# Performance work log

Hardware: AMD Instinct MI355X
Metric: run time of the kernel (lower is better)

## Reference

```python
import jax, jax.numpy as jnp
import numpy as np

N_HEADS = 16
EMBED = 1024
HEAD = EMBED // N_HEADS


def setup_inputs() -> dict:
    key = jax.random.key(0)
    k1, k2, k3, k4, k5 = jax.random.split(key, 5)
    x = jax.random.normal(k1, (2, 2048, EMBED), dtype=jnp.float32)
    # nn.Linear params: weight [out, in], bias [out]
    s_in = 1.0 / np.sqrt(EMBED)
    W_qkv = jax.random.uniform(k2, (3 * EMBED, EMBED), minval=-s_in, maxval=s_in, dtype=jnp.float32)
    b_qkv = jax.random.uniform(k3, (3 * EMBED,), minval=-s_in, maxval=s_in, dtype=jnp.float32)
    W_out = jax.random.uniform(k4, (EMBED, EMBED), minval=-s_in, maxval=s_in, dtype=jnp.float32)
    b_out = jax.random.uniform(k5, (EMBED,), minval=-s_in, maxval=s_in, dtype=jnp.float32)
    return {"x": x, "W_qkv": W_qkv, "b_qkv": b_qkv, "W_out": W_out, "b_out": b_out}


def reference(x, W_qkv, b_qkv, W_out, b_out):
    n, seq_len, _ = x.shape
    qkv = x @ W_qkv.T + b_qkv                       # [n, s, 3*E]
    q, k, v = jnp.split(qkv, 3, axis=2)
    def heads(t):
        return t.reshape(n, seq_len, N_HEADS, HEAD).transpose(0, 2, 1, 3)  # [n,h,s,d]
    q, k, v = heads(q), heads(k), heads(v)
    logits = jnp.einsum('bhqd,bhkd->bhqk', q, k) / jnp.sqrt(jnp.float32(HEAD))
    causal = jnp.tril(jnp.ones((seq_len, seq_len), dtype=bool))
    logits = jnp.where(causal[None, None], logits, -jnp.inf)
    attn = jax.nn.softmax(logits, axis=-1)
    o = jnp.einsum('bhqk,bhkd->bhqd', attn, v)      # [n,h,s,d]
    o = o.transpose(0, 2, 1, 3).reshape(n, seq_len, EMBED)
    return o @ W_out.T + b_out
```

## Files before the change

kernel.cpp:

```cpp
#include <hip/hip_runtime.h>
#include <hip/hip_bf16.h>
#include <stdint.h>

typedef unsigned short u16;
typedef unsigned int u32;
typedef __attribute__((ext_vector_type(8))) __bf16 bf16x8;
typedef __attribute__((ext_vector_type(8))) u16 u16x8;
typedef __attribute__((ext_vector_type(4))) u16 u16x4;
typedef __attribute__((ext_vector_type(4))) float f32x4;
typedef __attribute__((ext_vector_type(4))) u32 u32x4;
typedef __attribute__((ext_vector_type(2))) u32 u32x2;

#define S_LEN 2048
#define QSCALE 0.180336880f

__device__ __forceinline__ u16 f2bf(float f) {
  u32 u = __builtin_bit_cast(u32, f);
  u32 r = u + 0x7fffu + ((u >> 16) & 1u);
  return (u16)(r >> 16);
}
__device__ __forceinline__ float bf2f(u16 h) {
  u32 u = ((u32)h) << 16;
  return __builtin_bit_cast(float, u);
}
__device__ __forceinline__ float ex2(float x) { return __builtin_exp2f(x); }
__device__ __forceinline__ u32 cvtpk(float lo, float hi) {
  u32 d;
  asm("v_cvt_pk_bf16_f32 %0, %1, %2" : "=v"(d) : "v"(lo), "v"(hi));
  return d;
}

__device__ __forceinline__ void gload_lds16(const void* g, void* l) {
  __builtin_amdgcn_global_load_lds(
      (const __attribute__((address_space(1))) void*)g,
      (__attribute__((address_space(3))) void*)l, 16, 0, 0);
}

#define N4_X 1048576
#define N4_WQKV 786432
#define N4_WOUT 262144
__global__ void f2bf_all(const float* __restrict__ x, const float* __restrict__ wq,
                         const float* __restrict__ wo, u16* __restrict__ xb,
                         u16* __restrict__ wqb, u16* __restrict__ wob) {
  int i = blockIdx.x * blockDim.x + threadIdx.x;
  int stride = gridDim.x * blockDim.x;
  const int total = N4_X + N4_WQKV + N4_WOUT;
  for (; i < total; i += stride) {
    const float4* src; ushort4* dst; int k;
    if (i < N4_X) { src = (const float4*)x; dst = (ushort4*)xb; k = i; }
    else if (i < N4_X + N4_WQKV) { src = (const float4*)wq; dst = (ushort4*)wqb; k = i - N4_X; }
    else { src = (const float4*)wo; dst = (ushort4*)wob; k = i - N4_X - N4_WQKV; }
    float4 v = src[k];
    ushort4 o;
    o.x = f2bf(v.x); o.y = f2bf(v.y); o.z = f2bf(v.z); o.w = f2bf(v.w);
    dst[k] = o;
  }
}

template<int MODE, int XN>
__global__ __launch_bounds__(256) void gemm_bt(
    const u16* __restrict__ A, const u16* __restrict__ B,
    const float* __restrict__ bias, void* __restrict__ C0,
    u16* __restrict__ C1, int M, int N, int K, int ldc) {
  __shared__ __align__(16) u16 As[128 * 64];
  __shared__ __align__(16) u16 Bs[128 * 64];
  const int tid = threadIdx.x;
  const int wid = tid >> 6, lane = tid & 63;
  const int l15 = lane & 15, l4 = lane >> 4;
  const int wr = wid >> 1, wc = wid & 1;

  const int bid = blockIdx.x;
  const int xcd = bid & 7, s = bid >> 3;
  const int mtiles = M >> 7;
  const int nt = xcd * XN + s / mtiles;
  const int mt = s % mtiles;
  const int bm = mt * 128, bn = nt * 128;

  f32x4 acc[4][4] = {};

  for (int k0 = 0; k0 < K; k0 += 64) {
#pragma unroll
    for (int i = 0; i < 4; ++i) {
      int c = i * 256 + tid;
      int row = c >> 3, kc = c & 7;
      int sl = ((kc ^ (row & 7)) << 3);
      gload_lds16(A + (size_t)(bm + row) * K + k0 + sl, (char*)As + c * 16);
      gload_lds16(B + (size_t)(bn + row) * K + k0 + sl, (char*)Bs + c * 16);
    }
    __syncthreads();

#pragma unroll
    for (int kk = 0; kk < 2; ++kk) {
      bf16x8 a[4], b[4];
#pragma unroll
      for (int mi = 0; mi < 4; ++mi) {
        int row = wr * 64 + mi * 16 + l15;
        int slot = (kk * 4 + l4) ^ (row & 7);
        a[mi] = __builtin_bit_cast(bf16x8,
            *(const u32x4*)((char*)As + row * 128 + (slot << 4)));
      }
#pragma unroll
      for (int ni = 0; ni < 4; ++ni) {
        int row = wc * 64 + ni * 16 + l15;
        int slot = (kk * 4 + l4) ^ (row & 7);
        b[ni] = __builtin_bit_cast(bf16x8,
            *(const u32x4*)((char*)Bs + row * 128 + (slot << 4)));
      }
#pragma unroll
      for (int mi = 0; mi < 4; ++mi)
#pragma unroll
        for (int ni = 0; ni < 4; ++ni)
          acc[mi][ni] = __builtin_amdgcn_mfma_f32_16x16x32_bf16(
              a[mi], b[ni], acc[mi][ni], 0, 0, 0);
    }
    __syncthreads();
  }

#pragma unroll
  for (int ni = 0; ni < 4; ++ni) {
    int col = bn + wc * 64 + ni * 16 + l15;
    float bv = bias[col];
#pragma unroll
    for (int mi = 0; mi < 4; ++mi) {
      int row = bm + wr * 64 + mi * 16 + l4 * 4;
      if (MODE == 0) {
#pragma unroll
        for (int r = 0; r < 4; ++r)
          ((float*)C0)[(size_t)(row + r) * ldc + col] = acc[mi][ni][r] + bv;
      } else {
        if (col < 2048) {
          float sc = (col < 1024) ? QSCALE : 1.0f;
#pragma unroll
          for (int r = 0; r < 4; ++r)
            ((u16*)C0)[(size_t)(row + r) * 2048 + col] = f2bf((acc[mi][ni][r] + bv) * sc);
        } else {
          u16x4 vv;
#pragma unroll
          for (int r = 0; r < 4; ++r) vv[r] = f2bf(acc[mi][ni][r] + bv);
          int hh = (col - 2048) >> 6, d = (col - 2048) & 63;
          int bb = row >> 11, ss = row & 2047;
          *(u16x4*)&C1[(((size_t)(bb * 16 + hh) * 64 + d) << 11) + ss] = vv;
        }
      }
    }
  }
}

__global__ __launch_bounds__(256, 3) void attn13(
    const u16* __restrict__ qk, const u16* __restrict__ vt,
    u16* __restrict__ O, u16* __restrict__ pO, float* __restrict__ ML) {
  __shared__ __align__(16) u16 SM[3][2][64 * 64];
  __shared__ float MLsh[4][32];
  const int tid = threadIdx.x;
  const int wid = tid >> 6, lane = tid & 63;
  const int l15 = lane & 15, l4 = lane >> 4;
  const int qh = wid >> 1, kvh = wid & 1;

  const int bid = blockIdx.x;
  const int xcd = bid & 7, slot = bid >> 3;
  const int bh = xcd * 4 + slot / 48;
  const int i = slot % 48;
  const int b = bh >> 4, h = bh & 15;

  int qt, k0t, mode;
  if (i < 16)      { qt = 16 + i;  k0t = 0;  mode = 0; }
  else if (i < 32) { qt = 47 - i;  k0t = 16; mode = 1; }
  else             { qt = 47 - i;  k0t = 0;  mode = 2; }
  const int k1t = (mode == 0) ? 15 : qt;
  const int n = k1t - k0t + 1;

  const u16* qkb = qk + (((size_t)b * S_LEN) << 11);
  const u16* vtb = vt + ((size_t)bh << 17);
  const int qcol = h * 64, kcol = 1024 + h * 64;

  const int c0 = tid, c1 = 256 + tid;
  const int r0 = c0 >> 3, sw0 = ((c0 & 7) ^ (r0 & 7)) << 3;
  const int r1 = c1 >> 3, sw1 = ((c1 & 7) ^ (r1 & 7)) << 3;

  auto stage = [&](int buf, int kt) {
    int kvb = kt << 6;
    gload_lds16(qkb + (((size_t)(kvb + r0)) << 11) + kcol + sw0, (char*)&SM[buf][0][0] + c0 * 16);
    gload_lds16(qkb + (((size_t)(kvb + r1)) << 11) + kcol + sw1, (char*)&SM[buf][0][0] + c1 * 16);
    gload_lds16(vtb + ((size_t)r0 << 11) + kvb + sw0, (char*)&SM[buf][1][0] + c0 * 16);
    gload_lds16(vtb + ((size_t)r1 << 11) + kvb + sw1, (char*)&SM[buf][1][0] + c1 * 16);
  };

  bf16x8 qf[2][2];
#pragma unroll
  for (int qs = 0; qs < 2; ++qs)
#pragma unroll
    for (int kf = 0; kf < 2; ++kf) {
      int rq = qt * 64 + qh * 32 + qs * 16 + l15;
      qf[qs][kf] = __builtin_bit_cast(bf16x8,
          *(const u16x8*)&qkb[((size_t)rq << 11) + qcol + kf * 32 + l4 * 8]);
    }
  const int qpos0 = qt * 64 + qh * 32 + l15;

  float l_[2] = {0.f, 0.f};
  f32x4 o_[2][4] = {};

  stage(0, k0t);
  if (n > 1) stage(1, k0t + 1);

  for (int idx = 0; idx < n; ++idx) {
    const int kt = k0t + idx;
    const int kvb = kt << 6;
    if (idx == n - 1) asm volatile("s_waitcnt vmcnt(0)" ::: "memory");
    else              asm volatile("s_waitcnt vmcnt(4)" ::: "memory");
    __builtin_amdgcn_s_barrier();
    if (idx + 2 < n) stage((idx + 2) % 3, kt + 2);
    const int cur = idx % 3;

    const char* Kc = (const char*)&SM[cur][0][0];
    const char* Vc = (const char*)&SM[cur][1][0];

    f32x4 s[2][2] = {};
#pragma unroll
    for (int kf = 0; kf < 2; ++kf)
#pragma unroll
      for (int nt = 0; nt < 2; ++nt) {
        int row = kvh * 32 + nt * 16 + l15;
        int slot2 = (kf * 4 + l4) ^ (l15 & 7);
        bf16x8 kf8 = __builtin_bit_cast(bf16x8,
            *(const u32x4*)(Kc + row * 128 + (slot2 << 4)));
        s[0][nt] = __builtin_amdgcn_mfma_f32_16x16x32_bf16(kf8, qf[0][kf], s[0][nt], 0, 0, 0);
        s[1][nt] = __builtin_amdgcn_mfma_f32_16x16x32_bf16(kf8, qf[1][kf], s[1][nt], 0, 0, 0);
      }

    if (kt == qt) {
#pragma unroll
      for (int qs = 0; qs < 2; ++qs)
#pragma unroll
        for (int nt = 0; nt < 2; ++nt) {
          int kvr = kvb + kvh * 32 + nt * 16 + l4 * 4;
          int qp = qpos0 + qs * 16;
#pragma unroll
          for (int r = 0; r < 4; ++r)
            if (kvr + r > qp) s[qs][nt][r] = -__builtin_inff();
        }
    }

#pragma unroll
    for (int qs = 0; qs < 2; ++qs) {
#pragma unroll
      for (int nt = 0; nt < 2; ++nt)
#pragma unroll
        for (int r = 0; r < 4; ++r)
          s[qs][nt][r] = ex2(s[qs][nt][r]);
      l_[qs] += ((s[qs][0][0] + s[qs][0][1]) + (s[qs][0][2] + s[qs][0][3]))
              + ((s[qs][1][0] + s[qs][1][1]) + (s[qs][1][2] + s[qs][1][3]));
    }

    bf16x8 pa[2];
#pragma unroll
    for (int qs = 0; qs < 2; ++qs) {
      u32 w0 = cvtpk(s[qs][0][0], s[qs][0][1]);
      u32 w1 = cvtpk(s[qs][0][2], s[qs][0][3]);
      u32 w2 = cvtpk(s[qs][1][0], s[qs][1][1]);
      u32 w3 = cvtpk(s[qs][1][2], s[qs][1][3]);
      pa[qs] = __builtin_bit_cast(bf16x8, u32x4{w0, w1, w2, w3});
    }

    const int gc0 = kvh * 4 + (l4 >> 1);
    const int hb = (l4 & 1) * 8;
    const int sx = l15 & 7;
#pragma unroll
    for (int dt = 0; dt < 4; ++dt) {
      int d = dt * 16 + l15;
      const char* rowp = Vc + d * 128 + hb;
      u32x2 vlo = *(const u32x2*)(rowp + ((gc0 ^ sx) << 4));
      u32x2 vhi = *(const u32x2*)(rowp + (((gc0 + 2) ^ sx) << 4));
      bf16x8 vf = __builtin_bit_cast(bf16x8, u32x4{vlo[0], vlo[1], vhi[0], vhi[1]});
      o_[0][dt] = __builtin_amdgcn_mfma_f32_16x16x32_bf16(pa[0], vf, o_[0][dt], 0, 0, 0);
      o_[1][dt] = __builtin_amdgcn_mfma_f32_16x16x32_bf16(pa[1], vf, o_[1][dt], 0, 0, 0);
    }
  }

  float lt0 = l_[0] + __shfl_xor(l_[0], 16); lt0 += __shfl_xor(lt0, 32);
  float lt1 = l_[1] + __shfl_xor(l_[1], 16); lt1 += __shfl_xor(lt1, 32);

  __syncthreads();
  u16* pw = (u16*)SM + wid * 2048;
#pragma unroll
  for (int qs = 0; qs < 2; ++qs)
#pragma unroll
    for (int dt = 0; dt < 4; ++dt)
#pragma unroll
      for (int r = 0; r < 4; ++r)
        pw[(qs * 16 + l4 * 4 + r) * 64 + dt * 16 + l15] = f2bf(o_[qs][dt][r]);
  if (l4 == 0) {
    MLsh[wid][l15]      = lt0;
    MLsh[wid][16 + l15] = lt1;
  }
  __syncthreads();

  const int wA = (wid >> 1) << 1, wB = wA + 1;
  const u16* pA = (const u16*)SM + wA * 2048;
  const u16* pB = (const u16*)SM + wB * 2048;
  float inv[4], Lx[4];
  int qlr[4];
#pragma unroll
  for (int r = 0; r < 4; ++r) {
    int ql = (wid & 1) * 16 + l4 * 4 + r;
    qlr[r] = ql;
    float L = MLsh[wA][ql] + MLsh[wB][ql];
    Lx[r] = L;
    inv[r] = 1.0f / L;
  }

  if (mode == 2) {
#pragma unroll
    for (int dt = 0; dt < 4; ++dt)
#pragma unroll
      for (int r = 0; r < 4; ++r) {
        int idx2 = qlr[r] * 64 + dt * 16 + l15;
        float val = (bf2f(pA[idx2]) + bf2f(pB[idx2])) * inv[r];
        int tok = qt * 64 + wid * 16 + l4 * 4 + r;
        O[(((size_t)(b * S_LEN + tok)) << 10) + h * 64 + dt * 16 + l15] = f2bf(val);
      }
  } else {
    const int pslot = (((bh << 4) + (qt - 16)) << 1) + mode;
    u16* pb = pO + ((size_t)pslot << 12);
#pragma unroll
    for (int dt = 0; dt < 4; ++dt)
#pragma unroll
      for (int r = 0; r < 4; ++r) {
        int idx2 = qlr[r] * 64 + dt * 16 + l15;
        float val = (bf2f(pA[idx2]) + bf2f(pB[idx2])) * inv[r];
        int row = wid * 16 + l4 * 4 + r;
        pb[row * 64 + dt * 16 + l15] = f2bf(val);
      }
    if (l15 == 0) {
#pragma unroll
      for (int r = 0; r < 4; ++r) {
        int row = wid * 16 + l4 * 4 + r;
        ML[pslot * 128 + row] = Lx[r];
      }
    }
  }
}

__global__ __launch_bounds__(256) void combine(
    const u16* __restrict__ pO, const float* __restrict__ ML,
    u16* __restrict__ O) {
  const int qi = blockIdx.x, bh = blockIdx.y;
  const int b = bh >> 4, h = bh & 15;
  const int t = threadIdx.x;
  const int row = t >> 2, cblk = (t & 3) << 4;
  const int s0 = (((bh << 4) + qi) << 1), s1 = s0 + 1;
  float l0 = ML[s0 * 128 + row], l1 = ML[s1 * 128 + row];
  float inv = 1.0f / (l0 + l1);
  float w0 = l0 * inv, w1 = l1 * inv;
  const u16* p0 = pO + (((size_t)s0) << 12) + row * 64 + cblk;
  const u16* p1 = pO + (((size_t)s1) << 12) + row * 64 + cblk;
  const int tok = (16 + qi) * 64 + row;
  u16* dst = O + (((size_t)(b * S_LEN + tok)) << 10) + h * 64 + cblk;
#pragma unroll
  for (int half = 0; half < 2; ++half) {
    u16x8 a = *(const u16x8*)(p0 + half * 8);
    u16x8 c = *(const u16x8*)(p1 + half * 8);
    u16x8 o;
#pragma unroll
    for (int j = 0; j < 8; ++j)
      o[j] = f2bf(w0 * bf2f(a[j]) + w1 * bf2f(c[j]));
    *(u16x8*)(dst + half * 8) = o;
  }
}

extern "C" void kernel_launch(void* const* d_in, const int* in_sizes, int n_in,
                              void* d_out, int out_size, void* d_ws, size_t ws_size,
                              hipStream_t stream) {
  const float* x    = (const float*)d_in[0];
  const float* Wqkv = (const float*)d_in[1];
  const float* bqkv = (const float*)d_in[2];
  const float* Wout = (const float*)d_in[3];
  const float* bout = (const float*)d_in[4];
  float* out = (float*)d_out;

  u16* xb    = (u16*)d_ws;
  u16* wqkvb = xb + 4194304;
  u16* woutb = wqkvb + 3145728;
  u16* qkb   = woutb + 1048576;
  u16* vtb   = qkb + 8388608;
  u16* ob    = vtb + 4194304;
  u16*   pO = xb;
  float* ML = (float*)wqkvb;

  f2bf_all<<<2048, 256, 0, stream>>>(x, Wqkv, Wout, xb, wqkvb, woutb);

  gemm_bt<2, 3><<<dim3(768), 256, 0, stream>>>(xb, wqkvb, bqkv, qkb, vtb,
                                               4096, 3072, 1024, 0);
  attn13<<<dim3(1536), 256, 0, stream>>>(qkb, vtb, ob, pO, ML);
  combine<<<dim3(16, 32), 256, 0, stream>>>(pO, ML, ob);
  gemm_bt<0, 1><<<dim3(256), 256, 0, stream>>>(ob, woutb, bout, out, nullptr,
                                               4096, 1024, 1024, 1024);
}
```

Before: 114.6 us.

## Replace QKV projection GEMM with 256x256-tile triple-buffered 512-thread kernel

```diff
diff --git a/kernel.cpp b/kernel.cpp
--- a/kernel.cpp
+++ b/kernel.cpp
@@ -57,6 +57,95 @@
   }
 }
 
+__global__ __launch_bounds__(512, 1) void gemm256(
+    const u16* __restrict__ A, const u16* __restrict__ B,
+    const float* __restrict__ bias, u16* __restrict__ C0,
+    u16* __restrict__ C1, int K) {
+  __shared__ __align__(16) u16 As[3][256 * 32];
+  __shared__ __align__(16) u16 Bs[3][256 * 32];
+  const int tid = threadIdx.x;
+  const int lane = tid & 63, wid = tid >> 6;
+  const int l15 = lane & 15, l4 = lane >> 4;
+  const int wr = wid >> 2, wc = wid & 3;
+
+  const int bid = blockIdx.x;
+  const int xcd = bid & 7, s = bid >> 3;
+  const int idx0 = xcd * 24 + s;
+  const int nt = idx0 >> 4, mt = idx0 & 15;
+  const int bm = mt << 8, bn = nt << 8;
+
+  const int c0 = tid, c1 = 512 + tid;
+  const int r0 = c0 >> 2, k0c = ((c0 & 3) ^ (r0 & 3)) << 3;
+  const int r1 = c1 >> 2, k1c = ((c1 & 3) ^ (r1 & 3)) << 3;
+
+  auto stage = [&](int buf, int t) {
+    int kb = t << 5;
+    gload_lds16(A + (size_t)(bm + r0) * K + kb + k0c, (char*)&As[buf][0] + c0 * 16);
+    gload_lds16(A + (size_t)(bm + r1) * K + kb + k1c, (char*)&As[buf][0] + c1 * 16);
+    gload_lds16(B + (size_t)(bn + r0) * K + kb + k0c, (char*)&Bs[buf][0] + c0 * 16);
+    gload_lds16(B + (size_t)(bn + r1) * K + kb + k1c, (char*)&Bs[buf][0] + c1 * 16);
+  };
+
+  f32x4 acc[8][4] = {};
+  const int nsteps = K >> 5;
+
+  stage(0, 0);
+  stage(1, 1);
+  for (int t = 0; t < nsteps; ++t) {
+    if (t == nsteps - 1) asm volatile("s_waitcnt vmcnt(0)" ::: "memory");
+    else                 asm volatile("s_waitcnt vmcnt(4)" ::: "memory");
+    __builtin_amdgcn_s_barrier();
+    if (t + 2 < nsteps) stage((t + 2) % 3, t + 2);
+    const char* Ac = (const char*)&As[t % 3][0];
+    const char* Bc = (const char*)&Bs[t % 3][0];
+
+    bf16x8 a[8], b[4];
+#pragma unroll
+    for (int mi = 0; mi < 8; ++mi) {
+      int row = wr * 128 + mi * 16 + l15;
+      int slot = l4 ^ (row & 3);
+      a[mi] = __builtin_bit_cast(bf16x8,
+          *(const u32x4*)(Ac + row * 64 + (slot << 4)));
+    }
+#pragma unroll
+    for (int ni = 0; ni < 4; ++ni) {
+      int row = wc * 64 + ni * 16 + l15;
+      int slot = l4 ^ (row & 3);
+      b[ni] = __builtin_bit_cast(bf16x8,
+          *(const u32x4*)(Bc + row * 64 + (slot << 4)));
+    }
+#pragma unroll
+    for (int mi = 0; mi < 8; ++mi)
+#pragma unroll
+      for (int ni = 0; ni < 4; ++ni)
+        acc[mi][ni] = __builtin_amdgcn_mfma_f32_16x16x32_bf16(
+            a[mi], b[ni], acc[mi][ni], 0, 0, 0);
+  }
+
+#pragma unroll
+  for (int ni = 0; ni < 4; ++ni) {
+    int col = bn + wc * 64 + ni * 16 + l15;
+    float bv = bias[col];
+#pragma unroll
+    for (int mi = 0; mi < 8; ++mi) {
+      int row = bm + wr * 128 + mi * 16 + l4 * 4;
+      if (col < 2048) {
+        float sc = (col < 1024) ? QSCALE : 1.0f;
+#pragma unroll
+        for (int r = 0; r < 4; ++r)
+          C0[(size_t)(row + r) * 2048 + col] = f2bf((acc[mi][ni][r] + bv) * sc);
+      } else {
+        u16x4 vv;
+#pragma unroll
+        for (int r = 0; r < 4; ++r) vv[r] = f2bf(acc[mi][ni][r] + bv);
+        int hh = (col - 2048) >> 6, d = (col - 2048) & 63;
+        int bb = row >> 11, ss = row & 2047;
+        *(u16x4*)&C1[(((size_t)(bb * 16 + hh) * 64 + d) << 11) + ss] = vv;
+      }
+    }
+  }
+}
+
 template<int MODE, int XN>
 __global__ __launch_bounds__(256) void gemm_bt(
     const u16* __restrict__ A, const u16* __restrict__ B,
@@ -123,25 +212,9 @@
 #pragma unroll
     for (int mi = 0; mi < 4; ++mi) {
       int row = bm + wr * 64 + mi * 16 + l4 * 4;
-      if (MODE == 0) {
-#pragma unroll
-        for (int r = 0; r < 4; ++r)
-          ((float*)C0)[(size_t)(row + r) * ldc + col] = acc[mi][ni][r] + bv;
-      } else {
-        if (col < 2048) {
-          float sc = (col < 1024) ? QSCALE : 1.0f;
-#pragma unroll
-          for (int r = 0; r < 4; ++r)
-            ((u16*)C0)[(size_t)(row + r) * 2048 + col] = f2bf((acc[mi][ni][r] + bv) * sc);
-        } else {
-          u16x4 vv;
-#pragma unroll
-          for (int r = 0; r < 4; ++r) vv[r] = f2bf(acc[mi][ni][r] + bv);
-          int hh = (col - 2048) >> 6, d = (col - 2048) & 63;
-          int bb = row >> 11, ss = row & 2047;
-          *(u16x4*)&C1[(((size_t)(bb * 16 + hh) * 64 + d) << 11) + ss] = vv;
-        }
-      }
+#pragma unroll
+      for (int r = 0; r < 4; ++r)
+        ((float*)C0)[(size_t)(row + r) * ldc + col] = acc[mi][ni][r] + bv;
     }
   }
 }
@@ -154,7 +227,7 @@
   const int tid = threadIdx.x;
   const int wid = tid >> 6, lane = tid & 63;
   const int l15 = lane & 15, l4 = lane >> 4;
-  const int qh = wid >> 1, kvh = wid & 1;
+  const int kvh = wid & 1;
 
   const int bid = blockIdx.x;
   const int xcd = bid & 7, slot = bid >> 3;
@@ -190,11 +263,11 @@
   for (int qs = 0; qs < 2; ++qs)
 #pragma unroll
     for (int kf = 0; kf < 2; ++kf) {
-      int rq = qt * 64 + qh * 32 + qs * 16 + l15;
+      int rq = qt * 64 + (wid >> 1) * 32 + qs * 16 + l15;
       qf[qs][kf] = __builtin_bit_cast(bf16x8,
           *(const u16x8*)&qkb[((size_t)rq << 11) + qcol + kf * 32 + l4 * 8]);
     }
-  const int qpos0 = qt * 64 + qh * 32 + l15;
+  const int qpos0 = qt * 64 + (wid >> 1) * 32 + l15;
 
   float l_[2] = {0.f, 0.f};
   f32x4 o_[2][4] = {};
@@ -388,8 +461,7 @@
 
   f2bf_all<<<2048, 256, 0, stream>>>(x, Wqkv, Wout, xb, wqkvb, woutb);
 
-  gemm_bt<2, 3><<<dim3(768), 256, 0, stream>>>(xb, wqkvb, bqkv, qkb, vtb,
-                                               4096, 3072, 1024, 0);
+  gemm256<<<dim3(192), 512, 0, stream>>>(xb, wqkvb, bqkv, qkb, vtb, 1024);
   attn13<<<dim3(1536), 256, 0, stream>>>(qkb, vtb, ob, pO, ML);
   combine<<<dim3(16, 32), 256, 0, stream>>>(pO, ML, ob);
   gemm_bt<0, 1><<<dim3(256), 256, 0, stream>>>(ob, woutb, bout, out, nullptr,
```

Result: slower. 136.3 us (+18.9%).
